# Kernel optimization log

Measured on AMD Instinct MI355X. Metric: run time of the kernel, lower is better.

## Reference

```python
import jax, jax.numpy as jnp
import numpy as np

B, C, IN, OUT = 2048, 64, 512, 512


def setup_inputs() -> dict:
    key = jax.random.key(0)
    k1, k2, k3 = jax.random.split(key, 3)
    x = jax.random.normal(k1, (B, IN), dtype=jnp.float32)
    index = jax.random.randint(k2, (B,), 0, C, dtype=jnp.int64)
    # kaiming_uniform-ish init: bound = sqrt(6 / ((1 + 5) * fan_in)) = 1/sqrt(fan_in)
    bound = 1.0 / np.sqrt(IN)
    weight = jax.random.uniform(k3, (C, OUT, IN), dtype=jnp.float32,
                                minval=-bound, maxval=bound)
    return {"input": x, "index": index, "weight": weight}


def reference(input, index, weight):
    # weight: (C, OUT, IN); index: (B,); input: (B, IN)
    w = weight[index]                      # (B, OUT, IN) gathered per-sample matrix
    return jnp.einsum('boi,bi->bo', w, input)  # batched matvec -> (B, OUT)
```

## Files before the change

### kernel.cpp

```cpp
#include <hip/hip_runtime.h>


constexpr int Bsz  = 2048;
constexpr int Ccnt = 64;
constexpr int INF  = 512;
constexpr int OUTF = 512;
constexpr int THREADS = 256;
constexpr int OT = 32;
constexpr int NT = 64;
constexpr int NBLK = Ccnt * (OUTF / OT);

typedef __attribute__((ext_vector_type(8))) short bf16x8;
typedef __attribute__((ext_vector_type(4))) float f32x4;

#if __has_builtin(__builtin_amdgcn_cvt_pk_bf16_f32)
typedef __attribute__((ext_vector_type(2))) __bf16 bf16x2_t;
__device__ __forceinline__ int cvt2i(float a, float b) {
    union { bf16x2_t v; int i; } u;
    u.v = __builtin_amdgcn_cvt_pk_bf16_f32(a, b);
    return u.i;
}
#else
__device__ __forceinline__ unsigned f2bf(float f) {
    union { float f; unsigned u; } v; v.f = f;
    return (v.u + 0x7FFFu + ((v.u >> 16) & 1u)) >> 16;
}
__device__ __forceinline__ int cvt2i(float a, float b) {
    return (int)(f2bf(a) | (f2bf(b) << 16));
}
#endif

__device__ __forceinline__ bf16x8 cvt8(float4 a, float4 b) {
    union { bf16x8 v; int i[4]; } u;
    u.i[0] = cvt2i(a.x, a.y);
    u.i[1] = cvt2i(a.z, a.w);
    u.i[2] = cvt2i(b.x, b.y);
    u.i[3] = cvt2i(b.z, b.w);
    return u.v;
}

__device__ __forceinline__ void gld_lds16(const float* g, float* l) {
    __builtin_amdgcn_global_load_lds(
        (const __attribute__((address_space(1))) float*)g,
        (__attribute__((address_space(3))) float*)l, 16, 0, 0);
}

__global__ __launch_bounds__(THREADS, 2)
void switching_linear_kernel(const float* __restrict__ x,
                             const int* __restrict__ idx,
                             const float* __restrict__ w,
                             float* __restrict__ out) {
    __shared__ float Wl[OT * INF];
    __shared__ unsigned short list[Bsz];
    __shared__ int ls_n;

    const int tid  = threadIdx.x;
    const int wave = tid >> 6;
    const int lane = tid & 63;
    const int c  = blockIdx.x >> 4;
    const int o0 = (blockIdx.x & 15) * OT;

    if (tid == 0) ls_n = 0;
    __syncthreads();

    int myidx[8];
#pragma unroll
    for (int i = 0; i < 8; ++i) myidx[i] = idx[tid + i * THREADS];

    const float* wc = w + (size_t)c * OUTF * INF + (size_t)o0 * INF;
#pragma unroll
    for (int i = 0; i < 16; ++i) {
        const int inst = wave * 16 + i;
        const int ci = inst >> 1;
        const int h  = inst & 1;
        const int p  = h * 64 + lane;
        const int l  = p >> 1;
        const int row = (ci >> 4) * 16 + (l & 15);
        const int gk  = 2 * (l >> 4) + (p & 1);
        const float* src = wc + (size_t)row * INF + (ci & 15) * 32 + gk * 4;
        gld_lds16(src, &Wl[ci * 512 + h * 256]);
    }

#pragma unroll
    for (int i = 0; i < 8; ++i) {
        if (myidx[i] == c) list[atomicAdd(&ls_n, 1)] = (unsigned short)(tid + i * THREADS);
    }

    __syncthreads();
    const int n = ls_n;

    const int mrow = lane & 15;
    const int quad = lane >> 4;
    const int lofs = lane * 8;

    for (int s0 = 0; s0 < n; s0 += NT) {
        if (s0 + wave * 16 >= n) break;
        const int s = s0 + wave * 16 + mrow;
        const bool v = (s < n);
        const float* bp = x + (size_t)(v ? (int)list[s] : 0) * INF + quad * 8;

        f32x4 acc0 = {0.f,0.f,0.f,0.f}, acc1 = {0.f,0.f,0.f,0.f};

#pragma unroll 4
        for (int kt32 = 0; kt32 < 16; ++kt32) {
            const float* ch0 = &Wl[kt32 * 512 + lofs];
            const float* ch1 = &Wl[(16 + kt32) * 512 + lofs];
            float4 a00 = *(const float4*)ch0;
            float4 a01 = *(const float4*)(ch0 + 4);
            float4 a10 = *(const float4*)ch1;
            float4 a11 = *(const float4*)(ch1 + 4);

            bf16x8 bfr = {0,0,0,0,0,0,0,0};
            if (v) {
                float4 b0 = *(const float4*)(bp + kt32 * 32);
                float4 b1 = *(const float4*)(bp + kt32 * 32 + 4);
                bfr = cvt8(b0, b1);
            }
            acc0 = __builtin_amdgcn_mfma_f32_16x16x32_bf16(cvt8(a00, a01), bfr, acc0, 0, 0, 0);
            acc1 = __builtin_amdgcn_mfma_f32_16x16x32_bf16(cvt8(a10, a11), bfr, acc1, 0, 0, 0);
        }

        if (v) {
            float* d0 = out + (size_t)list[s] * OUTF + o0 + quad * 4;
            *(float4*)d0 = make_float4(acc0[0], acc0[1], acc0[2], acc0[3]);
            *(float4*)(d0 + 16) = make_float4(acc1[0], acc1[1], acc1[2], acc1[3]);
        }
    }
}

extern "C" void kernel_launch(void* const* d_in, const int* in_sizes, int n_in,
                              void* d_out, int out_size, void* d_ws, size_t ws_size,
                              hipStream_t stream) {
    const float* x   = (const float*)d_in[0];
    const int*   idx = (const int*)d_in[1];
    const float* w   = (const float*)d_in[2];
    float* out = (float*)d_out;

    switching_linear_kernel<<<dim3(NBLK), dim3(THREADS), 0, stream>>>(x, idx, w, out);
}
```

Measured before the change: 116.5 us.

## Keep per-wave weight tile in registers as bf16 instead of LDS staging

Each wave now owns a 16-row output slice and loads its weights straight from global memory into registers, converting them to bf16 once before the sample loop. This removes the LDS weight buffer and the repeated per-iteration LDS reads and conversions. Grid size drops to a quarter, with each block covering 64 output rows across 4 waves. Every wave now walks all samples of the class, so x rows are reloaded by each wave, and register pressure is higher.

```diff
diff --git a/kernel.cpp b/kernel.cpp
--- a/kernel.cpp
+++ b/kernel.cpp
@@ -6,9 +6,8 @@
 constexpr int INF  = 512;
 constexpr int OUTF = 512;
 constexpr int THREADS = 256;
-constexpr int OT = 32;
-constexpr int NT = 64;
-constexpr int NBLK = Ccnt * (OUTF / OT);
+constexpr int OT = 16;
+constexpr int NBLK = (Ccnt * (OUTF / OT)) / 4;
 
 typedef __attribute__((ext_vector_type(8))) short bf16x8;
 typedef __attribute__((ext_vector_type(4))) float f32x4;
@@ -39,91 +38,70 @@
     return u.v;
 }
 
-__device__ __forceinline__ void gld_lds16(const float* g, float* l) {
-    __builtin_amdgcn_global_load_lds(
-        (const __attribute__((address_space(1))) float*)g,
-        (__attribute__((address_space(3))) float*)l, 16, 0, 0);
-}
-
 __global__ __launch_bounds__(THREADS, 2)
 void switching_linear_kernel(const float* __restrict__ x,
                              const int* __restrict__ idx,
                              const float* __restrict__ w,
                              float* __restrict__ out) {
-    __shared__ float Wl[OT * INF];
     __shared__ unsigned short list[Bsz];
     __shared__ int ls_n;
 
     const int tid  = threadIdx.x;
     const int wave = tid >> 6;
     const int lane = tid & 63;
-    const int c  = blockIdx.x >> 4;
-    const int o0 = (blockIdx.x & 15) * OT;
+    const int c  = blockIdx.x >> 3;
+    const int o0 = ((blockIdx.x & 7) * 4 + wave) * OT;
+    const int mrow = lane & 15;
+    const int quad = lane >> 4;
 
     if (tid == 0) ls_n = 0;
     __syncthreads();
 
-    int myidx[8];
+    int my[8];
 #pragma unroll
-    for (int i = 0; i < 8; ++i) myidx[i] = idx[tid + i * THREADS];
+    for (int i = 0; i < 8; ++i) my[i] = idx[tid + i * THREADS];
 
-    const float* wc = w + (size_t)c * OUTF * INF + (size_t)o0 * INF;
+    const float* aptr = w + ((size_t)c * OUTF + (size_t)(o0 + mrow)) * INF + quad * 8;
+    float4 wv[32];
 #pragma unroll
-    for (int i = 0; i < 16; ++i) {
-        const int inst = wave * 16 + i;
-        const int ci = inst >> 1;
-        const int h  = inst & 1;
-        const int p  = h * 64 + lane;
-        const int l  = p >> 1;
-        const int row = (ci >> 4) * 16 + (l & 15);
-        const int gk  = 2 * (l >> 4) + (p & 1);
-        const float* src = wc + (size_t)row * INF + (ci & 15) * 32 + gk * 4;
-        gld_lds16(src, &Wl[ci * 512 + h * 256]);
+    for (int t = 0; t < 16; ++t) {
+        wv[2 * t]     = *(const float4*)(aptr + t * 32);
+        wv[2 * t + 1] = *(const float4*)(aptr + t * 32 + 4);
     }
 
 #pragma unroll
-    for (int i = 0; i < 8; ++i) {
-        if (myidx[i] == c) list[atomicAdd(&ls_n, 1)] = (unsigned short)(tid + i * THREADS);
-    }
+    for (int i = 0; i < 8; ++i)
+        if (my[i] == c) list[atomicAdd(&ls_n, 1)] = (unsigned short)(tid + i * THREADS);
 
     __syncthreads();
     const int n = ls_n;
 
-    const int mrow = lane & 15;
-    const int quad = lane >> 4;
-    const int lofs = lane * 8;
+    bf16x8 wf[16];
+#pragma unroll
+    for (int t = 0; t < 16; ++t) wf[t] = cvt8(wv[2 * t], wv[2 * t + 1]);
 
-    for (int s0 = 0; s0 < n; s0 += NT) {
-        if (s0 + wave * 16 >= n) break;
-        const int s = s0 + wave * 16 + mrow;
+    for (int g0 = 0; g0 < n; g0 += 16) {
+        const int s = g0 + mrow;
         const bool v = (s < n);
         const float* bp = x + (size_t)(v ? (int)list[s] : 0) * INF + quad * 8;
 
-        f32x4 acc0 = {0.f,0.f,0.f,0.f}, acc1 = {0.f,0.f,0.f,0.f};
-
-#pragma unroll 4
-        for (int kt32 = 0; kt32 < 16; ++kt32) {
-            const float* ch0 = &Wl[kt32 * 512 + lofs];
-            const float* ch1 = &Wl[(16 + kt32) * 512 + lofs];
-            float4 a00 = *(const float4*)ch0;
-            float4 a01 = *(const float4*)(ch0 + 4);
-            float4 a10 = *(const float4*)ch1;
-            float4 a11 = *(const float4*)(ch1 + 4);
-
-            bf16x8 bfr = {0,0,0,0,0,0,0,0};
+        f32x4 acc = {0.f, 0.f, 0.f, 0.f};
+#pragma unroll
+        for (int t = 0; t < 16; ++t) {
+            bf16x8 xf;
             if (v) {
-                float4 b0 = *(const float4*)(bp + kt32 * 32);
-                float4 b1 = *(const float4*)(bp + kt32 * 32 + 4);
-                bfr = cvt8(b0, b1);
+                float4 b0 = *(const float4*)(bp + t * 32);
+                float4 b1 = *(const float4*)(bp + t * 32 + 4);
+                xf = cvt8(b0, b1);
+            } else {
+                xf = (bf16x8){0, 0, 0, 0, 0, 0, 0, 0};
             }
-            acc0 = __builtin_amdgcn_mfma_f32_16x16x32_bf16(cvt8(a00, a01), bfr, acc0, 0, 0, 0);
-            acc1 = __builtin_amdgcn_mfma_f32_16x16x32_bf16(cvt8(a10, a11), bfr, acc1, 0, 0, 0);
+            acc = __builtin_amdgcn_mfma_f32_16x16x32_bf16(wf[t], xf, acc, 0, 0, 0);
         }
 
         if (v) {
-            float* d0 = out + (size_t)list[s] * OUTF + o0 + quad * 4;
-            *(float4*)d0 = make_float4(acc0[0], acc0[1], acc0[2], acc0[3]);
-            *(float4*)(d0 + 16) = make_float4(acc1[0], acc1[1], acc1[2], acc1[3]);
+            float* dst = out + (size_t)list[s] * OUTF + o0 + quad * 4;
+            *(float4*)dst = make_float4(acc[0], acc[1], acc[2], acc[3]);
         }
     }
 }
```

New measurement: 121.4 us. 1.04x slower.
